# Kernel optimization log

Measured on AMD Instinct MI355X. Metric: run time of the kernel, lower is better.

The kernel has to match this reference:

```python
import jax, jax.numpy as jnp
import numpy as np

N = 262144            # number of particles
H0 = 0.006            # base SPH support radius (unit square domain)
GRID = 256            # static upper bound on cells per dimension (actual ~170)
NUM_CELLS = GRID * GRID
K = 32                # max particles stored per cell (avg occupancy ~9.4)
NCAND = 9 * K         # searchRadius=1 -> 3x3 cell stencil
MAX_NEIGHBORS = 64    # padded neighbor-list width (avg neighbor count ~27)


def setup_inputs() -> dict:
    key = jax.random.key(0)
    kp, ks = jax.random.split(key)
    positions = jax.random.uniform(kp, (N, 2), dtype=jnp.float32)
    # supports in [0.9*H0, H0], mimicking mildly adaptive SPH supports
    supports = H0 * (0.9 + 0.1 * jax.random.uniform(ks, (N,), dtype=jnp.float32))
    return {"positions": positions, "supports": supports}


def _cell_linear_indices(positions, supports):
    # mirrors sortPositions: cell size = hMax, indices = ceil((p - qMin)/hMax)
    hMax = jnp.max(supports)
    qMin = jnp.min(positions, axis=0) - hMax
    ij = jnp.ceil((positions - qMin) / hMax).astype(jnp.int32)  # >= 1 by construction
    ij = jnp.clip(ij, 0, GRID - 1)
    return ij[:, 0] + GRID * ij[:, 1]


def _build_cell_table(lin):
    # dense equivalent of the hash-grid: sort by cell, counting-sort into [cell, slot]
    order = jnp.argsort(lin)                       # == sortingIndices in the original
    lin_s = lin[order]
    counts = jax.ops.segment_sum(jnp.ones(N, jnp.int32), lin, num_segments=NUM_CELLS)
    starts = jnp.cumsum(counts) - counts           # exclusive prefix sum == cumCell
    rank = jnp.arange(N, dtype=jnp.int32) - starts[lin_s].astype(jnp.int32)
    ovf = rank >= K                                # overflow slots -> dump row
    cell_t = jnp.where(ovf, NUM_CELLS, lin_s)
    slot_t = jnp.where(ovf, 0, rank)
    table = jnp.full((NUM_CELLS + 1, K), -1, dtype=jnp.int32)
    table = table.at[cell_t, slot_t].set(order.astype(jnp.int32))
    return table


def reference(positions, supports):
    lin = _cell_linear_indices(positions, supports)
    table = _build_cell_table(lin)

    # 3x3 stencil of neighbor cells (searchRadius = 1)
    dx, dy = jnp.meshgrid(jnp.arange(-1, 2), jnp.arange(-1, 2), indexing='ij')
    offs = (dx + GRID * dy).reshape(1, 9).astype(jnp.int32)
    cand_cells = jnp.clip(lin[:, None] + offs, 0, NUM_CELLS)  # [N, 9]

    cand = table[cand_cells].reshape(N, NCAND)     # [N, 288] candidate particle ids
    present = cand >= 0
    cidx = jnp.where(present, cand, 0)
    cpos = positions[cidx]                         # [N, 288, 2] gather (memory bound)
    diff = cpos - positions[:, None, :]
    dist = jnp.sqrt(jnp.sum(diff * diff, axis=-1)) # [N, 288]
    valid = present & (dist <= supports[:, None])  # |x_i - x_j| <= h_i (self included)
    count = jnp.sum(valid, axis=1).astype(jnp.int32)

    # compact valid candidates to the front, pad to MAX_NEIGHBORS
    order2 = jnp.argsort(jnp.where(valid, 0, 1).astype(jnp.int32), axis=1, stable=True)
    sel = order2[:, :MAX_NEIGHBORS]
    nbr = jnp.take_along_axis(cidx, sel, axis=1)
    dsel = jnp.take_along_axis(dist, sel, axis=1)
    inb = jnp.arange(MAX_NEIGHBORS)[None, :] < count[:, None]
    neighbors = jnp.where(inb, nbr, -1)
    radial = jnp.where(inb, dsel / supports[:, None], 0.0)  # fluidRadialDistances
    return neighbors, count, radial
```

## Files before the change

kernel.cpp:

```cpp
#include <hip/hip_runtime.h>
#include <float.h>

#define N_PART 262144
#define GRID_DIM 256
#define NUM_CELLS (GRID_DIM * GRID_DIM)
#define KP 32
#define MAXNB 64


__global__ __launch_bounds__(256) void prep_kernel(
        const float2* __restrict__ pos2, const float* __restrict__ sup,
        int* __restrict__ counts,
        float* __restrict__ bMinX, float* __restrict__ bMinY,
        float* __restrict__ bMaxH) {
    __shared__ unsigned s_minx, s_miny, s_maxh;
    int t = threadIdx.x, b = blockIdx.x;
    int tid = b * 256 + t;
    if (tid <= NUM_CELLS) counts[tid] = 0;
    if (t == 0) { s_minx = 0x7f7fffffu; s_miny = 0x7f7fffffu; s_maxh = 0u; }
    __syncthreads();
    float2 p = pos2[tid];
    float  h = sup[tid];
    atomicMin(&s_minx, __float_as_uint(p.x));
    atomicMin(&s_miny, __float_as_uint(p.y));
    atomicMax(&s_maxh, __float_as_uint(h));
    __syncthreads();
    if (t == 0) {
        bMinX[b] = __uint_as_float(s_minx);
        bMinY[b] = __uint_as_float(s_miny);
        bMaxH[b] = __uint_as_float(s_maxh);
    }
}

__global__ __launch_bounds__(256) void bin_kernel(
        const float2* __restrict__ pos2,
        const float* __restrict__ bMinX, const float* __restrict__ bMinY,
        const float* __restrict__ bMaxH,
        int* __restrict__ counts, int* __restrict__ tableA) {
    __shared__ unsigned s_minx, s_miny, s_maxh;
    int t = threadIdx.x;
    int tid = blockIdx.x * 256 + t;
    if (t == 0) { s_minx = 0x7f7fffffu; s_miny = 0x7f7fffffu; s_maxh = 0u; }
    __syncthreads();
    {
        float mx = FLT_MAX, my = FLT_MAX, mh = 0.0f;
        for (int k = t; k < 1024; k += 256) {
            mx = fminf(mx, bMinX[k]);
            my = fminf(my, bMinY[k]);
            mh = fmaxf(mh, bMaxH[k]);
        }
        atomicMin(&s_minx, __float_as_uint(mx));
        atomicMin(&s_miny, __float_as_uint(my));
        atomicMax(&s_maxh, __float_as_uint(mh));
    }
    __syncthreads();
    float hmax  = __uint_as_float(s_maxh);
    float qminx = __uint_as_float(s_minx) - hmax;
    float qminy = __uint_as_float(s_miny) - hmax;
    float2 p = pos2[tid];
    int cx = (int)ceilf((p.x - qminx) / hmax);
    int cy = (int)ceilf((p.y - qminy) / hmax);
    cx = min(max(cx, 0), GRID_DIM - 1);
    cy = min(max(cy, 0), GRID_DIM - 1);
    int c = cx + GRID_DIM * cy;
    int slot = atomicAdd(&counts[c], 1);
    if (slot < KP) tableA[(c << 5) + slot] = tid;
}

__global__ __launch_bounds__(256) void rank_kernel(
        const float2* __restrict__ pos2, const float* __restrict__ sup,
        const int* __restrict__ counts, const int* __restrict__ tableA,
        float4* __restrict__ Qpad, int* __restrict__ linR,
        int4* __restrict__ cinfo) {
    int tid = blockIdx.x * 256 + threadIdx.x;
    int c   = tid >> 3;
    int s0  = tid & 7;
    int cnt = min(counts[c], KP);
    const int* row = tableA + (c << 5);
    for (int sl = s0; sl < cnt; sl += 8) {
        int id = row[sl];
        int rank = 0;
        for (int k = 0; k < cnt; k++) rank += (row[k] < id);
        float2 p = pos2[id];
        float  h = sup[id];
        float  hn  = __int_as_float(__float_as_int(h) + 1);
        double mid = 0.5 * ((double)h + (double)hn);
        double t2  = mid * mid;
        float  S   = (float)t2;
        S = ((double)S > t2) ? __int_as_float(__float_as_int(S) - 1) : S;
        Qpad[(c << 5) + rank] = make_float4(p.x, p.y, __int_as_float(id), S);
        linR[id] = (c << 5) | rank;
    }
    if (s0 == 0) {
        const int offs[9] = {-257, -1, 255, -256, 0, 256, -255, 1, 257};
        int cum = 0;
        int v[9];
#pragma unroll
        for (int o = 0; o < 9; o++) {
            int cl = min(max(c + offs[o], 0), NUM_CELLS);
            cum += min(counts[cl], KP);
            v[o] = cum;
        }
        cinfo[c * 3 + 0] = make_int4(v[0], v[1], v[2], v[3]);
        cinfo[c * 3 + 1] = make_int4(v[4], v[5], v[6], v[7]);
        cinfo[c * 3 + 2] = make_int4(v[8], 0, 0, 0);
    }
}

__global__ __launch_bounds__(256) void query_kernel(
        const int* __restrict__ linR, const int4* __restrict__ cinfo,
        const float4* __restrict__ Qpad,
        float* __restrict__ outN, float* __restrict__ outC,
        float* __restrict__ outR) {
#pragma clang fp contract(off)
    __shared__ int   s_id[4][MAXNB];
    __shared__ float s_s2[4][MAXNB];

    int t    = threadIdx.x;
    int lane = t & 63;
    int wsl  = t >> 6;
    int bid  = blockIdx.x;
    int swz  = (bid & 7) * (int)(gridDim.x >> 3) + (bid >> 3);
    int w    = __builtin_amdgcn_readfirstlane(swz * 4 + wsl);

    int lr = __builtin_amdgcn_readfirstlane(linR[w]);
    int c  = lr >> 5;

    int4 ca = cinfo[c * 3 + 0];
    int4 cb = cinfo[c * 3 + 1];
    int4 cz = cinfo[c * 3 + 2];
    float4 me = Qpad[lr];
    float px = me.x, py = me.y, S = me.w;

    const int offs[9] = {-257, -1, 255, -256, 0, 256, -255, 1, 257};
    int cum[10] = {0, ca.x, ca.y, ca.z, ca.w, cb.x, cb.y, cb.z, cb.w, };
    cum[9] = cz.x;
    int T = cum[9];
    int delta[9];
#pragma unroll
    for (int o = 0; o < 9; o++) {
        int cl = min(max(c + offs[o], 0), NUM_CELLS);
        delta[o] = (cl << 5) - cum[o];
    }

    if (T <= 64) {
        int dsel = delta[0];
#pragma unroll
        for (int m = 1; m < 9; m++)
            dsel = (lane >= cum[m]) ? delta[m] : dsel;
        int idx = (lane < T) ? (lane + dsel) : lr;
        float4 q = Qpad[idx];
        unsigned long long maskT = (T >= 64) ? ~0ull : ((1ull << T) - 1ull);
        float dx = q.x - px;
        float dy = q.y - py;
        float s2 = dx * dx + dy * dy;
        bool keep = (s2 <= S) && (lane < T);
        unsigned long long bal = __ballot(s2 <= S) & maskT;
        int rank = __builtin_amdgcn_mbcnt_hi(
            (unsigned)(bal >> 32),
            __builtin_amdgcn_mbcnt_lo((unsigned)bal, 0));
        if (keep) {
            s_id[wsl][rank] = __float_as_int(q.z);
            s_s2[wsl][rank] = s2;
        }
        int total = (int)__popcll(bal);
        int   jj = s_id[wsl][lane];
        float ss = s_s2[wsl][lane];
        bool inb = lane < total;
        float rh = __builtin_amdgcn_rsqf(S);
        float vN = inb ? (float)jj : -1.0f;
        float vR = inb ? __builtin_amdgcn_sqrtf(ss) * rh : 0.0f;
        size_t base = (size_t)w * MAXNB;
        outN[base + lane] = vN;
        outR[base + lane] = vR;
        if (lane == 0) outC[w] = (float)total;
    } else {
        int total = 0;
        for (int b0 = 0; b0 < T; b0 += 64) {
            int ll = b0 + lane;
            int dsel = delta[0];
#pragma unroll
            for (int m = 1; m < 9; m++)
                dsel = (ll >= cum[m]) ? delta[m] : dsel;
            float4 q = Qpad[ll + dsel];
            float dx = q.x - px;
            float dy = q.y - py;
            float s2 = dx * dx + dy * dy;
            int rem = T - b0;
            unsigned long long maskT =
                (rem >= 64) ? ~0ull : ((1ull << rem) - 1ull);
            unsigned long long bal = __ballot(s2 <= S) & maskT;
            int rank = __builtin_amdgcn_mbcnt_hi(
                (unsigned)(bal >> 32),
                __builtin_amdgcn_mbcnt_lo((unsigned)bal, 0));
            int ww = total + rank;
            if ((s2 <= S) && (ll < T) && (ww < MAXNB)) {
                s_id[wsl][ww] = __float_as_int(q.z);
                s_s2[wsl][ww] = s2;
            }
            total += (int)__popcll(bal);
        }
        int stored = min(total, MAXNB);
        int   jj = s_id[wsl][lane];
        float ss = s_s2[wsl][lane];
        bool inb = lane < stored;
        float rh = __builtin_amdgcn_rsqf(S);
        float vN = inb ? (float)jj : -1.0f;
        float vR = inb ? __builtin_amdgcn_sqrtf(ss) * rh : 0.0f;
        size_t base = (size_t)w * MAXNB;
        outN[base + lane] = vN;
        outR[base + lane] = vR;
        if (lane == 0) outC[w] = (float)total;
    }
}

extern "C" void kernel_launch(void* const* d_in, const int* in_sizes, int n_in,
                              void* d_out, int out_size, void* d_ws, size_t ws_size,
                              hipStream_t stream) {
    const float2* pos2 = (const float2*)d_in[0];
    const float*  sup  = (const float*)d_in[1];

    char* p = (char*)d_ws;
    auto alloc = [&](size_t bytes) {
        char* q = p;
        p += (bytes + 255) & ~(size_t)255;
        return q;
    };
    int*    counts = (int*)alloc((size_t)(NUM_CELLS + 1) * 4);
    float*  bMinX  = (float*)alloc(1024 * 4);
    float*  bMinY  = (float*)alloc(1024 * 4);
    float*  bMaxH  = (float*)alloc(1024 * 4);
    int*    tableA = (int*)alloc((size_t)(NUM_CELLS + 1) * KP * 4);
    float4* Qpad   = (float4*)alloc(((size_t)(NUM_CELLS + 1) * KP + 64) * 16);
    int*    linR   = (int*)alloc((size_t)N_PART * 4);
    int4*   cinfo  = (int4*)alloc((size_t)NUM_CELLS * 3 * 16);

    float* out  = (float*)d_out;
    float* outN = out;
    float* outC = out + (size_t)N_PART * MAXNB;
    float* outR = outC + N_PART;

    prep_kernel<<<N_PART / 256, 256, 0, stream>>>(pos2, sup, counts,
                                                  bMinX, bMinY, bMaxH);
    bin_kernel<<<N_PART / 256, 256, 0, stream>>>(pos2, bMinX, bMinY, bMaxH,
                                                 counts, tableA);
    rank_kernel<<<NUM_CELLS * 8 / 256, 256, 0, stream>>>(pos2, sup, counts,
                                                         tableA, Qpad, linR,
                                                         cinfo);
    query_kernel<<<N_PART / 4, 256, 0, stream>>>(linR, cinfo, Qpad,
                                                 outN, outC, outR);
}
```

Measured before the change: 267.4 us.

## Recompute query cell and support radius in query kernel instead of storing linR

The query kernel now reads its particle's position and support directly, recomputes the cell index from bounds stored in a small params buffer, and derives the squared-radius threshold itself. This removes the linR array and the per-particle sup read and S computation from the rank kernel, cutting its scattered writes. The cinfo stride is padded from 3 to 4 int4 entries per cell for shift-based indexing. The cost is extra per-wave arithmetic, including a double-precision step, in the query kernel, plus an unsorted read of pos2/sup by wave index.

```diff
diff --git a/kernel.cpp b/kernel.cpp
--- a/kernel.cpp
+++ b/kernel.cpp
@@ -36,6 +36,7 @@
         const float2* __restrict__ pos2,
         const float* __restrict__ bMinX, const float* __restrict__ bMinY,
         const float* __restrict__ bMaxH,
+        unsigned* __restrict__ params,
         int* __restrict__ counts, int* __restrict__ tableA) {
     __shared__ unsigned s_minx, s_miny, s_maxh;
     int t = threadIdx.x;
@@ -54,6 +55,9 @@
         atomicMax(&s_maxh, __float_as_uint(mh));
     }
     __syncthreads();
+    if (blockIdx.x == 0 && t == 0) {
+        params[0] = s_minx; params[1] = s_miny; params[2] = s_maxh;
+    }
     float hmax  = __uint_as_float(s_maxh);
     float qminx = __uint_as_float(s_minx) - hmax;
     float qminy = __uint_as_float(s_miny) - hmax;
@@ -68,10 +72,9 @@
 }
 
 __global__ __launch_bounds__(256) void rank_kernel(
-        const float2* __restrict__ pos2, const float* __restrict__ sup,
+        const float2* __restrict__ pos2,
         const int* __restrict__ counts, const int* __restrict__ tableA,
-        float4* __restrict__ Qpad, int* __restrict__ linR,
-        int4* __restrict__ cinfo) {
+        float4* __restrict__ Qpad, int4* __restrict__ cinfo) {
     int tid = blockIdx.x * 256 + threadIdx.x;
     int c   = tid >> 3;
     int s0  = tid & 7;
@@ -82,14 +85,7 @@
         int rank = 0;
         for (int k = 0; k < cnt; k++) rank += (row[k] < id);
         float2 p = pos2[id];
-        float  h = sup[id];
-        float  hn  = __int_as_float(__float_as_int(h) + 1);
-        double mid = 0.5 * ((double)h + (double)hn);
-        double t2  = mid * mid;
-        float  S   = (float)t2;
-        S = ((double)S > t2) ? __int_as_float(__float_as_int(S) - 1) : S;
-        Qpad[(c << 5) + rank] = make_float4(p.x, p.y, __int_as_float(id), S);
-        linR[id] = (c << 5) | rank;
+        Qpad[(c << 5) + rank] = make_float4(p.x, p.y, __int_as_float(id), 0.0f);
     }
     if (s0 == 0) {
         const int offs[9] = {-257, -1, 255, -256, 0, 256, -255, 1, 257};
@@ -101,15 +97,16 @@
             cum += min(counts[cl], KP);
             v[o] = cum;
         }
-        cinfo[c * 3 + 0] = make_int4(v[0], v[1], v[2], v[3]);
-        cinfo[c * 3 + 1] = make_int4(v[4], v[5], v[6], v[7]);
-        cinfo[c * 3 + 2] = make_int4(v[8], 0, 0, 0);
+        cinfo[(c << 2) + 0] = make_int4(v[0], v[1], v[2], v[3]);
+        cinfo[(c << 2) + 1] = make_int4(v[4], v[5], v[6], v[7]);
+        cinfo[(c << 2) + 2] = make_int4(v[8], 0, 0, 0);
     }
 }
 
 __global__ __launch_bounds__(256) void query_kernel(
-        const int* __restrict__ linR, const int4* __restrict__ cinfo,
-        const float4* __restrict__ Qpad,
+        const float2* __restrict__ pos2, const float* __restrict__ sup,
+        const unsigned* __restrict__ params,
+        const int4* __restrict__ cinfo, const float4* __restrict__ Qpad,
         float* __restrict__ outN, float* __restrict__ outC,
         float* __restrict__ outR) {
 #pragma clang fp contract(off)
@@ -123,14 +120,30 @@
     int swz  = (bid & 7) * (int)(gridDim.x >> 3) + (bid >> 3);
     int w    = __builtin_amdgcn_readfirstlane(swz * 4 + wsl);
 
-    int lr = __builtin_amdgcn_readfirstlane(linR[w]);
-    int c  = lr >> 5;
-
-    int4 ca = cinfo[c * 3 + 0];
-    int4 cb = cinfo[c * 3 + 1];
-    int4 cz = cinfo[c * 3 + 2];
-    float4 me = Qpad[lr];
-    float px = me.x, py = me.y, S = me.w;
+    float2 pw = pos2[w];
+    float  h  = sup[w];
+    float px = __int_as_float(__builtin_amdgcn_readfirstlane(__float_as_int(pw.x)));
+    float py = __int_as_float(__builtin_amdgcn_readfirstlane(__float_as_int(pw.y)));
+    h = __int_as_float(__builtin_amdgcn_readfirstlane(__float_as_int(h)));
+
+    float hmax  = __uint_as_float(params[2]);
+    float qminx = __uint_as_float(params[0]) - hmax;
+    float qminy = __uint_as_float(params[1]) - hmax;
+    int cx = (int)ceilf((px - qminx) / hmax);
+    int cy = (int)ceilf((py - qminy) / hmax);
+    cx = min(max(cx, 0), GRID_DIM - 1);
+    cy = min(max(cy, 0), GRID_DIM - 1);
+    int c = __builtin_amdgcn_readfirstlane(cx + GRID_DIM * cy);
+
+    float  hn  = __int_as_float(__float_as_int(h) + 1);
+    double mid = 0.5 * ((double)h + (double)hn);
+    double t2  = mid * mid;
+    float  S   = (float)t2;
+    S = ((double)S > t2) ? __int_as_float(__float_as_int(S) - 1) : S;
+
+    int4 ca = cinfo[(c << 2) + 0];
+    int4 cb = cinfo[(c << 2) + 1];
+    int4 cz = cinfo[(c << 2) + 2];
 
     const int offs[9] = {-257, -1, 255, -256, 0, 256, -255, 1, 257};
     int cum[10] = {0, ca.x, ca.y, ca.z, ca.w, cb.x, cb.y, cb.z, cb.w, };
@@ -148,7 +161,7 @@
 #pragma unroll
         for (int m = 1; m < 9; m++)
             dsel = (lane >= cum[m]) ? delta[m] : dsel;
-        int idx = (lane < T) ? (lane + dsel) : lr;
+        int idx = (lane < T) ? (lane + dsel) : (c << 5);
         float4 q = Qpad[idx];
         unsigned long long maskT = (T >= 64) ? ~0ull : ((1ull << T) - 1ull);
         float dx = q.x - px;
@@ -226,14 +239,14 @@
         p += (bytes + 255) & ~(size_t)255;
         return q;
     };
+    unsigned* params = (unsigned*)alloc(256);
     int*    counts = (int*)alloc((size_t)(NUM_CELLS + 1) * 4);
     float*  bMinX  = (float*)alloc(1024 * 4);
     float*  bMinY  = (float*)alloc(1024 * 4);
     float*  bMaxH  = (float*)alloc(1024 * 4);
     int*    tableA = (int*)alloc((size_t)(NUM_CELLS + 1) * KP * 4);
     float4* Qpad   = (float4*)alloc(((size_t)(NUM_CELLS + 1) * KP + 64) * 16);
-    int*    linR   = (int*)alloc((size_t)N_PART * 4);
-    int4*   cinfo  = (int4*)alloc((size_t)NUM_CELLS * 3 * 16);
+    int4*   cinfo  = (int4*)alloc((size_t)NUM_CELLS * 4 * 16);
 
     float* out  = (float*)d_out;
     float* outN = out;
@@ -243,10 +256,9 @@
     prep_kernel<<<N_PART / 256, 256, 0, stream>>>(pos2, sup, counts,
                                                   bMinX, bMinY, bMaxH);
     bin_kernel<<<N_PART / 256, 256, 0, stream>>>(pos2, bMinX, bMinY, bMaxH,
-                                                 counts, tableA);
-    rank_kernel<<<NUM_CELLS * 8 / 256, 256, 0, stream>>>(pos2, sup, counts,
-                                                         tableA, Qpad, linR,
-                                                         cinfo);
-    query_kernel<<<N_PART / 4, 256, 0, stream>>>(linR, cinfo, Qpad,
-                                                 outN, outC, outR);
-}
+                                                 params, counts, tableA);
+    rank_kernel<<<NUM_CELLS * 8 / 256, 256, 0, stream>>>(pos2, counts,
+                                                         tableA, Qpad, cinfo);
+    query_kernel<<<N_PART / 4, 256, 0, stream>>>(pos2, sup, params, cinfo,
+                                                 Qpad, outN, outC, outR);
+}
```

Result: no change. 271.2 us (+1.4%).
